# Performance work log

Measured on AMD Instinct MI355X. Metric: run time of the kernel, lower is better.

## Reference

```python
import jax, jax.numpy as jnp
import numpy as np

D = 64
H = 4
HD = D // H
N_MOL, E_MOL = 2048, 32768
N_PROT, E_PROT = 8192, 262144
LN_EPS = 1e-5


def _lin_params(key, d_in, d_out):
    k1, k2 = jax.random.split(key)
    lim = 1.0 / np.sqrt(d_in)
    w = jax.random.uniform(k1, (d_in, d_out), minval=-lim, maxval=lim, dtype=jnp.float32)
    b = jax.random.uniform(k2, (d_out,), minval=-lim, maxval=lim, dtype=jnp.float32)
    return w, b


def setup_inputs() -> dict:
    key = jax.random.key(0)
    ks = jax.random.split(key, 20)
    inp = {
        'x_mol': jax.random.normal(ks[0], (N_MOL, D), dtype=jnp.float32),
        'edge_index_mol': jax.random.randint(ks[1], (2, E_MOL), 0, N_MOL),
        'edge_attr_mol': jax.random.normal(ks[2], (E_MOL, D), dtype=jnp.float32),
        'x_prot': jax.random.normal(ks[3], (N_PROT, D), dtype=jnp.float32),
        'edge_index_prot': jax.random.randint(ks[4], (2, E_PROT), 0, N_PROT),
        'edge_attr_prot': jax.random.normal(ks[5], (E_PROT, D), dtype=jnp.float32),
    }
    # GINE MLPs: Linear -> ReLU -> Linear
    inp['mol_w1'], inp['mol_b1'] = _lin_params(ks[6], D, D)
    inp['mol_w2'], inp['mol_b2'] = _lin_params(ks[7], D, D)
    inp['prot_w1'], inp['prot_b1'] = _lin_params(ks[8], D, D)
    inp['prot_w2'], inp['prot_b2'] = _lin_params(ks[9], D, D)
    # cross-attn mol->prot (query=mol, key/value=prot)
    inp['mp_wq'], inp['mp_bq'] = _lin_params(ks[10], D, D)
    inp['mp_wk'], inp['mp_bk'] = _lin_params(ks[11], D, D)
    inp['mp_wv'], inp['mp_bv'] = _lin_params(ks[12], D, D)
    # cross-attn prot->mol (query=prot, key/value=mol)
    inp['pm_wq'], inp['pm_bq'] = _lin_params(ks[13], D, D)
    inp['pm_wk'], inp['pm_bk'] = _lin_params(ks[14], D, D)
    inp['pm_wv'], inp['pm_bv'] = _lin_params(ks[15], D, D)
    # layer norms
    inp['ln_mol_g'] = jnp.ones((D,), jnp.float32)
    inp['ln_mol_b'] = jnp.zeros((D,), jnp.float32)
    inp['ln_prot_g'] = jnp.ones((D,), jnp.float32)
    inp['ln_prot_b'] = jnp.zeros((D,), jnp.float32)
    return inp


def _gine_conv(x, edge_index, edge_attr, w1, b1, w2, b2, n_nodes):
    # message: relu(x_j + edge_attr); aggregate: mean at target; update: MLP((1+eps)*x + aggr), eps=0
    src, dst = edge_index[0], edge_index[1]
    msg = jax.nn.relu(x[src] + edge_attr)                       # [E, D]
    ssum = jax.ops.segment_sum(msg, dst, num_segments=n_nodes)  # [N, D]
    cnt = jax.ops.segment_sum(jnp.ones((msg.shape[0],), msg.dtype), dst, num_segments=n_nodes)
    aggr = ssum / jnp.maximum(cnt, 1.0)[:, None]
    h = x + aggr
    h = jax.nn.relu(h @ w1 + b1) @ w2 + b2
    return h


def _cross_attn(q_nodes, k_nodes, wq, bq, wk, bk, wv, bv):
    Nq, Nk = q_nodes.shape[0], k_nodes.shape[0]
    Q = (q_nodes @ wq + bq).reshape(Nq, H, HD)
    K = (k_nodes @ wk + bk).reshape(Nk, H, HD)
    V = (k_nodes @ wv + bv).reshape(Nk, H, HD)
    scores = jnp.einsum('qhd,khd->hqk', Q, K) / np.sqrt(HD).astype(np.float32)
    attn = jax.nn.softmax(scores, axis=-1)                      # [H, Nq, Nk]
    out = jnp.einsum('hqk,khd->qhd', attn, V).reshape(Nq, D)
    return out


def _layer_norm(x, g, b):
    mu = jnp.mean(x, axis=-1, keepdims=True)
    var = jnp.mean(jnp.square(x - mu), axis=-1, keepdims=True)
    return (x - mu) * jax.lax.rsqrt(var + LN_EPS) * g + b


def reference(x_mol, edge_index_mol, edge_attr_mol, x_prot, edge_index_prot, edge_attr_prot,
              mol_w1, mol_b1, mol_w2, mol_b2, prot_w1, prot_b1, prot_w2, prot_b2,
              mp_wq, mp_bq, mp_wk, mp_bk, mp_wv, mp_bv,
              pm_wq, pm_bq, pm_wk, pm_bk, pm_wv, pm_bv,
              ln_mol_g, ln_mol_b, ln_prot_g, ln_prot_b):
    h_mol = jax.nn.relu(_gine_conv(x_mol, edge_index_mol, edge_attr_mol,
                                   mol_w1, mol_b1, mol_w2, mol_b2, x_mol.shape[0]))
    h_prot = jax.nn.relu(_gine_conv(x_prot, edge_index_prot, edge_attr_prot,
                                    prot_w1, prot_b1, prot_w2, prot_b2, x_prot.shape[0]))
    h_mol_attn = _cross_attn(h_mol, h_prot, mp_wq, mp_bq, mp_wk, mp_bk, mp_wv, mp_bv)
    h_prot_attn = _cross_attn(h_prot, h_mol, pm_wq, pm_bq, pm_wk, pm_bk, pm_wv, pm_bv)
    out_mol = _layer_norm(h_mol + h_mol_attn, ln_mol_g, ln_mol_b)
    out_prot = _layer_norm(h_prot + h_prot_attn, ln_prot_g, ln_prot_b)
    return out_mol, out_prot
```

## Files before the change

### kernel.cpp

```cpp
#include <hip/hip_runtime.h>

#define NM 2048
#define EM 32768
#define NP 8192
#define EP 262144

typedef __attribute__((ext_vector_type(8))) short short8;
typedef __attribute__((ext_vector_type(4))) float f32x4;

#define LOG2E 1.44269504088896340736f

__device__ __forceinline__ float e2(float x) { return __builtin_amdgcn_exp2f(x); }
__device__ __forceinline__ unsigned int pk_bf16(float a, float b) {
    unsigned int ua = __float_as_uint(a) + 0x8000u;
    unsigned int ub = __float_as_uint(b) + 0x8000u;
    return __builtin_amdgcn_perm(ua, ub, 0x03020706u);
}
__device__ __forceinline__ unsigned short cvt_bf16(float f) {
    unsigned int u = __float_as_uint(f);
    u = (u + 0x7fff + ((u >> 16) & 1)) >> 16;
    return (unsigned short)u;
}

__global__ __launch_bounds__(256) void hist_kernel(
    const int* __restrict__ ei_m, const int* __restrict__ ei_p,
    int* __restrict__ cnt_m, int* __restrict__ cnt_p)
{
    int idx = blockIdx.x * 256 + threadIdx.x;
    if (idx < EM) atomicAdd(&cnt_m[ei_m[EM + idx]], 1);
    int j = idx - EM;
    if (j >= 0 && j < EP) atomicAdd(&cnt_p[ei_p[EP + j]], 1);
}

__global__ __launch_bounds__(256) void scan_kernel(
    const int* __restrict__ cnt_m, const int* __restrict__ cnt_p,
    int* __restrict__ start_m, int* __restrict__ start_p,
    int* __restrict__ cur_m, int* __restrict__ cur_p)
{
    const int* cnt; int* start; int* cur; int n;
    if (blockIdx.x == 0) { cnt = cnt_m; start = start_m; cur = cur_m; n = NM; }
    else                 { cnt = cnt_p; start = start_p; cur = cur_p; n = NP; }
    int per = n >> 8;
    int tid = threadIdx.x;
    int base = tid * per;
    int s = 0;
    for (int i = 0; i < per; i++) s += cnt[base + i];
    __shared__ int wsum[4];
    int lane = tid & 63, w = tid >> 6;
    int v = s;
    #pragma unroll
    for (int off = 1; off < 64; off <<= 1) {
        int u = __shfl_up(v, off, 64);
        if (lane >= off) v += u;
    }
    if (lane == 63) wsum[w] = v;
    __syncthreads();
    int wo = 0;
    for (int i = 0; i < w; i++) wo += wsum[i];
    int run = wo + v - s;
    for (int i = 0; i < per; i++) {
        start[base + i] = run; cur[base + i] = run;
        run += cnt[base + i];
    }
    if (tid == 255) start[n] = run;
}

__global__ __launch_bounds__(256) void scatter_kernel(
    const int* __restrict__ ei_m, const int* __restrict__ ei_p,
    int* __restrict__ cur_m, int* __restrict__ cur_p,
    int* __restrict__ pidx_m, int* __restrict__ pidx_p)
{
    int idx = blockIdx.x * 256 + threadIdx.x;
    if (idx < EM) {
        int d = ei_m[EM + idx];
        int pos = atomicAdd(&cur_m[d], 1);
        pidx_m[pos] = (idx << 11) | ei_m[idx];
    }
    int j = idx - EM;
    if (j >= 0 && j < EP) {
        int d = ei_p[EP + j];
        int pos = atomicAdd(&cur_p[d], 1);
        pidx_p[pos] = (j << 13) | ei_p[j];
    }
}

__global__ __launch_bounds__(256) void node_aggr_kernel(
    const float* __restrict__ x_m, const float* __restrict__ ea_m,
    const int* __restrict__ start_m, const int* __restrict__ pidx_m,
    const float* __restrict__ x_p, const float* __restrict__ ea_p,
    const int* __restrict__ start_p, const int* __restrict__ pidx_p,
    float* __restrict__ h0_m, float* __restrict__ h0_p)
{
    int wave = threadIdx.x >> 6, lane = threadIdx.x & 63;
    int nid = blockIdx.x * 4 + wave;
    const float *x, *ea; const int *start, *pidx; float* h0; int n, sh, msk;
    if (nid < NM) { x = x_m; ea = ea_m; start = start_m; pidx = pidx_m; h0 = h0_m; n = nid; sh = 11; msk = 2047; }
    else          { x = x_p; ea = ea_p; start = start_p; pidx = pidx_p; h0 = h0_p; n = nid - NM; sh = 13; msk = 8191; }
    int b = start[n], e = start[n + 1];
    int deg = e - b;
    float acc = 0.f;
    for (int c0 = 0; c0 < deg; c0 += 64) {
        int rem = deg - c0;
        int mcount = rem < 64 ? rem : 64;
        int pk = 0;
        if (lane < mcount) pk = pidx[b + c0 + lane];
        int j = 0;
        for (; j + 3 < mcount; j += 4) {
            int v0 = __shfl(pk, j, 64),     v1 = __shfl(pk, j + 1, 64);
            int v2 = __shfl(pk, j + 2, 64), v3 = __shfl(pk, j + 3, 64);
            float a0 = ea[(size_t)(((unsigned)v0) >> sh) * 64 + lane];
            float a1 = ea[(size_t)(((unsigned)v1) >> sh) * 64 + lane];
            float a2 = ea[(size_t)(((unsigned)v2) >> sh) * 64 + lane];
            float a3 = ea[(size_t)(((unsigned)v3) >> sh) * 64 + lane];
            float y0 = x[(size_t)(v0 & msk) * 64 + lane];
            float y1 = x[(size_t)(v1 & msk) * 64 + lane];
            float y2 = x[(size_t)(v2 & msk) * 64 + lane];
            float y3 = x[(size_t)(v3 & msk) * 64 + lane];
            acc += fmaxf(y0 + a0, 0.f);
            acc += fmaxf(y1 + a1, 0.f);
            acc += fmaxf(y2 + a2, 0.f);
            acc += fmaxf(y3 + a3, 0.f);
        }
        for (; j < mcount; ++j) {
            int v0 = __shfl(pk, j, 64);
            acc += fmaxf(x[(size_t)(v0 & msk) * 64 + lane] + ea[(size_t)(((unsigned)v0) >> sh) * 64 + lane], 0.f);
        }
    }
    float aggr = acc / fmaxf((float)deg, 1.f);
    h0[(size_t)n * 64 + lane] = x[(size_t)n * 64 + lane] + aggr;
}

__global__ __launch_bounds__(256) void gine_mlp_kernel(
    const float* __restrict__ h0_m, const float* __restrict__ h0_p,
    const float* __restrict__ w1m, const float* __restrict__ b1m,
    const float* __restrict__ w2m, const float* __restrict__ b2m,
    const float* __restrict__ w1p, const float* __restrict__ b1p,
    const float* __restrict__ w2p, const float* __restrict__ b2p,
    float* __restrict__ hm, float* __restrict__ hp)
{
    const float *h0, *w1, *b1, *w2, *b2; float* out; int row0;
    if (blockIdx.x < NM / 16) {
        h0 = h0_m; w1 = w1m; b1 = b1m; w2 = w2m; b2 = b2m; out = hm;
        row0 = blockIdx.x * 16;
    } else {
        h0 = h0_p; w1 = w1p; b1 = b1p; w2 = w2p; b2 = b2p; out = hp;
        row0 = (blockIdx.x - NM / 16) * 16;
    }
    __shared__ float sW1[4096], sW2[4096], sb1[64], sb2[64];
    __shared__ float sh0[16][64], sh1[16][64];
    int t = threadIdx.x;
    for (int i = t; i < 4096; i += 256) { sW1[i] = w1[i]; sW2[i] = w2[i]; }
    if (t < 64) { sb1[t] = b1[t]; sb2[t] = b2[t]; }
    for (int i = t; i < 16 * 64; i += 256) {
        int r = i >> 6, c = i & 63;
        sh0[r][c] = h0[(size_t)(row0 + r) * 64 + c];
    }
    __syncthreads();
    int j = t & 63, rs = t >> 6;
    for (int r = rs; r < 16; r += 4) {
        float a = sb1[j];
        #pragma unroll
        for (int c = 0; c < 64; c++) a += sh0[r][c] * sW1[c * 64 + j];
        sh1[r][j] = fmaxf(a, 0.0f);
    }
    __syncthreads();
    for (int r = rs; r < 16; r += 4) {
        float a = sb2[j];
        #pragma unroll
        for (int c = 0; c < 64; c++) a += sh1[r][c] * sW2[c * 64 + j];
        out[(size_t)(row0 + r) * 64 + j] = fmaxf(a, 0.0f);
    }
}

__global__ __launch_bounds__(256) void qkv_bf16_kernel(
    const float* __restrict__ hm, const float* __restrict__ hp,
    const float* __restrict__ wq_m, const float* __restrict__ bq_m,
    const float* __restrict__ wk_m, const float* __restrict__ bk_m,
    const float* __restrict__ wv_m, const float* __restrict__ bv_m,
    const float* __restrict__ wq_p, const float* __restrict__ bq_p,
    const float* __restrict__ wk_p, const float* __restrict__ bk_p,
    const float* __restrict__ wv_p, const float* __restrict__ bv_p,
    unsigned short* __restrict__ Qm, unsigned short* __restrict__ Km, unsigned short* __restrict__ Vtm,
    unsigned short* __restrict__ Qp, unsigned short* __restrict__ Kp, unsigned short* __restrict__ Vtp)
{
    const float *x, *wq, *bq, *wk, *bk, *wv, *bv;
    unsigned short *Q, *K, *Vt; int row0, N;
    if (blockIdx.x < NM / 16) {
        x = hm; wq = wq_m; bq = bq_m; wk = wk_m; bk = bk_m; wv = wv_m; bv = bv_m;
        Q = Qm; K = Km; Vt = Vtm; N = NM; row0 = blockIdx.x * 16;
    } else {
        x = hp; wq = wq_p; bq = bq_p; wk = wk_p; bk = bk_p; wv = wv_p; bv = bv_p;
        Q = Qp; K = Kp; Vt = Vtp; N = NP; row0 = (blockIdx.x - NM / 16) * 16;
    }
    __shared__ float sWq[4096], sWk[4096], sWv[4096];
    __shared__ float sbq[64], sbk[64], sbv[64];
    __shared__ float sh0[16][64];
    int t = threadIdx.x;
    for (int i = t; i < 4096; i += 256) { sWq[i] = wq[i]; sWk[i] = wk[i]; sWv[i] = wv[i]; }
    if (t < 64) { sbq[t] = bq[t]; sbk[t] = bk[t]; sbv[t] = bv[t]; }
    for (int i = t; i < 16 * 64; i += 256) {
        int r = i >> 6, c = i & 63;
        sh0[r][c] = x[(size_t)(row0 + r) * 64 + c];
    }
    __syncthreads();
    int j = t & 63, rs = t >> 6;
    for (int r = rs; r < 16; r += 4) {
        float aq = sbq[j], ak = sbk[j], av = sbv[j];
        #pragma unroll
        for (int c = 0; c < 64; c++) {
            float h = sh0[r][c];
            aq += h * sWq[c * 64 + j];
            ak += h * sWk[c * 64 + j];
            av += h * sWv[c * 64 + j];
        }
        size_t o = (size_t)(row0 + r) * 64 + j;
        Q[o] = cvt_bf16(aq * (0.25f * LOG2E));
        K[o] = cvt_bf16(ak);
        Vt[(size_t)j * N + row0 + r] = cvt_bf16(av);
    }
}

__global__ __launch_bounds__(256) void attn_kernel(
    const unsigned short* __restrict__ Qm, const unsigned short* __restrict__ Km,
    const unsigned short* __restrict__ Vtm,
    const unsigned short* __restrict__ Qp, const unsigned short* __restrict__ Kp,
    const unsigned short* __restrict__ Vtp,
    float* __restrict__ partial)
{
    __shared__ unsigned int plds[4][16][20];
    int t = threadIdx.x;
    int wave = t >> 6;
    int lane = t & 63;
    int qrow = lane & 15;
    int quad = lane >> 4;
    int T = blockIdx.x * 4 + wave;

    const unsigned short *Q, *K, *Vt; int Nk, ncb, tloc;
    if (T < 4096) { Q = Qm; K = Kp; Vt = Vtp; Nk = NP; ncb = 3; tloc = T; }
    else          { Q = Qp; K = Km; Vt = Vtm; Nk = NM; ncb = 1; tloc = T - 4096; }
    int chunk = tloc & ((1 << ncb) - 1);
    int tmp = tloc >> ncb;
    int h = tmp & 3;
    int qt = tmp >> 2;

    short8 qf = {};
    if (quad < 2)
        qf = *(const short8*)(Q + ((size_t)(qt * 16 + qrow)) * 64 + h * 16 + quad * 8);

    float m = -3.0e38f, l = 0.0f;
    f32x4 acc = {0.f, 0.f, 0.f, 0.f};
    const f32x4 zero4 = {0.f, 0.f, 0.f, 0.f};
    int kbase = chunk * 1024;
    const unsigned short* vrow = Vt + ((size_t)(h * 16 + qrow)) * Nk;

    short8 kf0n = {}, kf1n = {}, vfn;
    {
        if (quad < 2) {
            kf0n = *(const short8*)(K + ((size_t)(kbase + qrow)) * 64 + h * 16 + quad * 8);
            kf1n = *(const short8*)(K + ((size_t)(kbase + 16 + qrow)) * 64 + h * 16 + quad * 8);
        }
        vfn = *(const short8*)(vrow + kbase + quad * 8);
    }

    for (int it = 0; it < 32; ++it) {
        short8 kf0 = kf0n, kf1 = kf1n, vf = vfn;
        if (it < 31) {
            int key0 = kbase + (it + 1) * 32;
            if (quad < 2) {
                kf0n = *(const short8*)(K + ((size_t)(key0 + qrow)) * 64 + h * 16 + quad * 8);
                kf1n = *(const short8*)(K + ((size_t)(key0 + 16 + qrow)) * 64 + h * 16 + quad * 8);
            }
            vfn = *(const short8*)(vrow + key0 + quad * 8);
        }

        f32x4 s0 = __builtin_amdgcn_mfma_f32_16x16x32_bf16(kf0, qf, zero4, 0, 0, 0);
        f32x4 s1 = __builtin_amdgcn_mfma_f32_16x16x32_bf16(kf1, qf, zero4, 0, 0, 0);

        float tmax = fmaxf(fmaxf(fmaxf(s0.x, s0.y), fmaxf(s0.z, s0.w)),
                           fmaxf(fmaxf(s1.x, s1.y), fmaxf(s1.z, s1.w)));
        tmax = fmaxf(tmax, __shfl_xor(tmax, 16, 64));
        tmax = fmaxf(tmax, __shfl_xor(tmax, 32, 64));
        float mnew = fmaxf(m, tmax);
        float alpha = e2(m - mnew);
        float p00 = e2(s0.x - mnew), p01 = e2(s0.y - mnew);
        float p02 = e2(s0.z - mnew), p03 = e2(s0.w - mnew);
        float p10 = e2(s1.x - mnew), p11 = e2(s1.y - mnew);
        float p12 = e2(s1.z - mnew), p13 = e2(s1.w - mnew);
        l = l * alpha + (((p00 + p01) + (p02 + p03)) + ((p10 + p11) + (p12 + p13)));
        acc.x *= alpha; acc.y *= alpha; acc.z *= alpha; acc.w *= alpha;

        uint2 w0; w0.x = pk_bf16(p00, p01); w0.y = pk_bf16(p02, p03);
        uint2 w1; w1.x = pk_bf16(p10, p11); w1.y = pk_bf16(p12, p13);
        *(uint2*)&plds[wave][qrow][quad * 2] = w0;
        *(uint2*)&plds[wave][qrow][8 + quad * 2] = w1;
        short8 pf = *(short8*)&plds[wave][qrow][quad * 4];

        acc = __builtin_amdgcn_mfma_f32_16x16x32_bf16(vf, pf, acc, 0, 0, 0);
        m = mnew;
    }

    float ltot = l + __shfl_xor(l, 16, 64);
    ltot += __shfl_xor(ltot, 32, 64);

    float* pb = partial + (size_t)T * 288;
    *(f32x4*)&pb[qrow * 16 + quad * 4] = acc;
    if (quad == 0) { pb[256 + qrow] = m; pb[272 + qrow] = ltot; }
}

__global__ __launch_bounds__(256) void merge_ln_kernel(
    const float* __restrict__ partial,
    const float* __restrict__ h_m, const float* __restrict__ h_p,
    const float* __restrict__ gm, const float* __restrict__ bm,
    const float* __restrict__ gp, const float* __restrict__ bp_,
    float* __restrict__ out)
{
    int t = threadIdx.x;
    int grow = blockIdx.x * 4 + (t >> 6);
    int c = t & 63;
    const float *pbase, *hbuf, *g, *bb; float* o; int NC, row;
    if (grow < NM) { pbase = partial;               hbuf = h_m; g = gm; bb = bm;  o = out;             NC = 8; row = grow; }
    else           { pbase = partial + 4096 * 288;  hbuf = h_p; g = gp; bb = bp_; o = out + NM * 64;   NC = 2; row = grow - NM; }
    int hi = c >> 4, d = c & 15;
    int qt = row >> 4, ql = row & 15;
    const float* base = pbase + (size_t)(qt * 4 + hi) * NC * 288;
    float M = -3.0e38f;
    for (int cc = 0; cc < NC; ++cc) M = fmaxf(M, base[cc * 288 + 256 + ql]);
    float L = 0.0f, A = 0.0f;
    for (int cc = 0; cc < NC; ++cc) {
        float w = e2(base[cc * 288 + 256 + ql] - M);
        L += base[cc * 288 + 272 + ql] * w;
        A += base[cc * 288 + ql * 16 + d] * w;
    }
    float v = hbuf[(size_t)row * 64 + c] + A / L;
    float s = v;
    #pragma unroll
    for (int o2 = 32; o2 >= 1; o2 >>= 1) s += __shfl_xor(s, o2, 64);
    float mu = s * (1.0f / 64.0f);
    float dv = v - mu;
    float sq = dv * dv;
    #pragma unroll
    for (int o2 = 32; o2 >= 1; o2 >>= 1) sq += __shfl_xor(sq, o2, 64);
    float var = sq * (1.0f / 64.0f);
    o[(size_t)row * 64 + c] = dv * rsqrtf(var + 1e-5f) * g[c] + bb[c];
}

extern "C" void kernel_launch(void* const* d_in, const int* in_sizes, int n_in,
                              void* d_out, int out_size, void* d_ws, size_t ws_size,
                              hipStream_t stream)
{
    const float* x_mol   = (const float*)d_in[0];
    const int*   ei_mol  = (const int*)  d_in[1];
    const float* ea_mol  = (const float*)d_in[2];
    const float* x_prot  = (const float*)d_in[3];
    const int*   ei_prot = (const int*)  d_in[4];
    const float* ea_prot = (const float*)d_in[5];
    const float* mol_w1  = (const float*)d_in[6];
    const float* mol_b1  = (const float*)d_in[7];
    const float* mol_w2  = (const float*)d_in[8];
    const float* mol_b2  = (const float*)d_in[9];
    const float* prot_w1 = (const float*)d_in[10];
    const float* prot_b1 = (const float*)d_in[11];
    const float* prot_w2 = (const float*)d_in[12];
    const float* prot_b2 = (const float*)d_in[13];
    const float* mp_wq = (const float*)d_in[14]; const float* mp_bq = (const float*)d_in[15];
    const float* mp_wk = (const float*)d_in[16]; const float* mp_bk = (const float*)d_in[17];
    const float* mp_wv = (const float*)d_in[18]; const float* mp_bv = (const float*)d_in[19];
    const float* pm_wq = (const float*)d_in[20]; const float* pm_bq = (const float*)d_in[21];
    const float* pm_wk = (const float*)d_in[22]; const float* pm_bk = (const float*)d_in[23];
    const float* pm_wv = (const float*)d_in[24]; const float* pm_bv = (const float*)d_in[25];
    const float* ln_mol_g  = (const float*)d_in[26];
    const float* ln_mol_b  = (const float*)d_in[27];
    const float* ln_prot_g = (const float*)d_in[28];
    const float* ln_prot_b = (const float*)d_in[29];

    float* ws = (float*)d_ws;
    float* h_mol   = ws;
    float* h_prot  = h_mol + 131072;
    float* partial = h_prot + 524288;
    float* h0_mol  = partial;
    float* h0_prot = h0_mol + 131072;
    int* ip      = (int*)(partial + 2359296);
    int* cnt_m   = ip;
    int* cnt_p   = cnt_m + 2048;
    int* start_m = cnt_p + 8192;
    int* start_p = start_m + 2052;
    int* cur_m   = start_p + 8196;
    int* cur_p   = cur_m + 2048;
    int* pidx_m  = cur_p + 8192;
    int* pidx_p  = pidx_m + 32768;
    unsigned short* bf = (unsigned short*)(pidx_p + 262144);
    unsigned short* Qm  = bf;
    unsigned short* Km  = Qm + 131072;
    unsigned short* Vtm = Km + 131072;
    unsigned short* Qp  = Vtm + 131072;
    unsigned short* Kp  = Qp + 524288;
    unsigned short* Vtp = Kp + 524288;

    hipMemsetAsync(cnt_m, 0, (size_t)(2048 + 8192) * sizeof(int), stream);

    const int EB = (EM + EP) / 256;
    hist_kernel<<<EB, 256, 0, stream>>>(ei_mol, ei_prot, cnt_m, cnt_p);
    scan_kernel<<<2, 256, 0, stream>>>(cnt_m, cnt_p, start_m, start_p, cur_m, cur_p);
    scatter_kernel<<<EB, 256, 0, stream>>>(ei_mol, ei_prot, cur_m, cur_p, pidx_m, pidx_p);
    node_aggr_kernel<<<(NM + NP) / 4, 256, 0, stream>>>(
        x_mol, ea_mol, start_m, pidx_m,
        x_prot, ea_prot, start_p, pidx_p, h0_mol, h0_prot);

    gine_mlp_kernel<<<(NM + NP) / 16, 256, 0, stream>>>(
        h0_mol, h0_prot, mol_w1, mol_b1, mol_w2, mol_b2,
        prot_w1, prot_b1, prot_w2, prot_b2, h_mol, h_prot);

    qkv_bf16_kernel<<<(NM + NP) / 16, 256, 0, stream>>>(
        h_mol, h_prot,
        mp_wq, mp_bq, pm_wk, pm_bk, pm_wv, pm_bv,
        pm_wq, pm_bq, mp_wk, mp_bk, mp_wv, mp_bv,
        Qm, Km, Vtm, Qp, Kp, Vtp);

    attn_kernel<<<2048, 256, 0, stream>>>(Qm, Km, Vtm, Qp, Kp, Vtp, partial);

    float* out = (float*)d_out;
    merge_ln_kernel<<<(NM + NP) / 4, 256, 0, stream>>>(
        partial, h_mol, h_prot, ln_mol_g, ln_mol_b, ln_prot_g, ln_prot_b, out);
}
```

Measured before the change: 323.3 us.

## Use Cauchy-Schwarz static softmax max, deeper K/V prefetch, float4 edge gather

Node aggregation now processes four edges per wave at once with float4 loads per lane, then reduces across lane groups, replacing the per-lane scalar gather. The QKV kernel computes per-row Q and K norms and atomically records global maxima. Attention uses the product of those maxima as a fixed softmax offset, removing the online max, rescaling and cross-lane max shuffles. K/V prefetch is deepened to two stages with double-buffered P in LDS. The fixed offset is a loose upper bound and can cause exp underflow in bf16 and fp32 when scores sit far below it, which risks accuracy, and it adds atomics plus a global dependency between kernels.

```diff
diff --git a/kernel.cpp b/kernel.cpp
--- a/kernel.cpp
+++ b/kernel.cpp
@@ -92,42 +92,44 @@
     float* __restrict__ h0_m, float* __restrict__ h0_p)
 {
     int wave = threadIdx.x >> 6, lane = threadIdx.x & 63;
+    int slot = lane >> 4, dq = lane & 15;
     int nid = blockIdx.x * 4 + wave;
     const float *x, *ea; const int *start, *pidx; float* h0; int n, sh, msk;
     if (nid < NM) { x = x_m; ea = ea_m; start = start_m; pidx = pidx_m; h0 = h0_m; n = nid; sh = 11; msk = 2047; }
     else          { x = x_p; ea = ea_p; start = start_p; pidx = pidx_p; h0 = h0_p; n = nid - NM; sh = 13; msk = 8191; }
     int b = start[n], e = start[n + 1];
     int deg = e - b;
-    float acc = 0.f;
-    for (int c0 = 0; c0 < deg; c0 += 64) {
-        int rem = deg - c0;
-        int mcount = rem < 64 ? rem : 64;
-        int pk = 0;
-        if (lane < mcount) pk = pidx[b + c0 + lane];
-        int j = 0;
-        for (; j + 3 < mcount; j += 4) {
-            int v0 = __shfl(pk, j, 64),     v1 = __shfl(pk, j + 1, 64);
-            int v2 = __shfl(pk, j + 2, 64), v3 = __shfl(pk, j + 3, 64);
-            float a0 = ea[(size_t)(((unsigned)v0) >> sh) * 64 + lane];
-            float a1 = ea[(size_t)(((unsigned)v1) >> sh) * 64 + lane];
-            float a2 = ea[(size_t)(((unsigned)v2) >> sh) * 64 + lane];
-            float a3 = ea[(size_t)(((unsigned)v3) >> sh) * 64 + lane];
-            float y0 = x[(size_t)(v0 & msk) * 64 + lane];
-            float y1 = x[(size_t)(v1 & msk) * 64 + lane];
-            float y2 = x[(size_t)(v2 & msk) * 64 + lane];
-            float y3 = x[(size_t)(v3 & msk) * 64 + lane];
-            acc += fmaxf(y0 + a0, 0.f);
-            acc += fmaxf(y1 + a1, 0.f);
-            acc += fmaxf(y2 + a2, 0.f);
-            acc += fmaxf(y3 + a3, 0.f);
+    const int* pp = pidx + b;
+    float4 acc = {0.f, 0.f, 0.f, 0.f};
+    for (int j = 0; j < deg; j += 4) {
+        int jj = j + slot;
+        if (jj < deg) {
+            int v = pp[jj];
+            const float4 a = *(const float4*)(ea + (size_t)(((unsigned)v) >> sh) * 64 + dq * 4);
+            const float4 y = *(const float4*)(x + (size_t)(v & msk) * 64 + dq * 4);
+            acc.x += fmaxf(y.x + a.x, 0.f);
+            acc.y += fmaxf(y.y + a.y, 0.f);
+            acc.z += fmaxf(y.z + a.z, 0.f);
+            acc.w += fmaxf(y.w + a.w, 0.f);
         }
-        for (; j < mcount; ++j) {
-            int v0 = __shfl(pk, j, 64);
-            acc += fmaxf(x[(size_t)(v0 & msk) * 64 + lane] + ea[(size_t)(((unsigned)v0) >> sh) * 64 + lane], 0.f);
-        }
-    }
-    float aggr = acc / fmaxf((float)deg, 1.f);
-    h0[(size_t)n * 64 + lane] = x[(size_t)n * 64 + lane] + aggr;
+    }
+    #pragma unroll
+    for (int off = 16; off <= 32; off <<= 1) {
+        acc.x += __shfl_xor(acc.x, off, 64);
+        acc.y += __shfl_xor(acc.y, off, 64);
+        acc.z += __shfl_xor(acc.z, off, 64);
+        acc.w += __shfl_xor(acc.w, off, 64);
+    }
+    if (slot == 0) {
+        float dinv = 1.0f / fmaxf((float)deg, 1.0f);
+        const float4 xv = *(const float4*)(x + (size_t)n * 64 + dq * 4);
+        float4 o;
+        o.x = xv.x + acc.x * dinv;
+        o.y = xv.y + acc.y * dinv;
+        o.z = xv.z + acc.z * dinv;
+        o.w = xv.w + acc.w * dinv;
+        *(float4*)(h0 + (size_t)n * 64 + dq * 4) = o;
+    }
 }
 
 __global__ __launch_bounds__(256) void gine_mlp_kernel(
@@ -181,20 +183,22 @@
     const float* __restrict__ wk_p, const float* __restrict__ bk_p,
     const float* __restrict__ wv_p, const float* __restrict__ bv_p,
     unsigned short* __restrict__ Qm, unsigned short* __restrict__ Km, unsigned short* __restrict__ Vtm,
-    unsigned short* __restrict__ Qp, unsigned short* __restrict__ Kp, unsigned short* __restrict__ Vtp)
+    unsigned short* __restrict__ Qp, unsigned short* __restrict__ Kp, unsigned short* __restrict__ Vtp,
+    int* __restrict__ norms)
 {
     const float *x, *wq, *bq, *wk, *bk, *wv, *bv;
-    unsigned short *Q, *K, *Vt; int row0, N;
+    unsigned short *Q, *K, *Vt; int row0, N, nbase;
     if (blockIdx.x < NM / 16) {
         x = hm; wq = wq_m; bq = bq_m; wk = wk_m; bk = bk_m; wv = wv_m; bv = bv_m;
-        Q = Qm; K = Km; Vt = Vtm; N = NM; row0 = blockIdx.x * 16;
+        Q = Qm; K = Km; Vt = Vtm; N = NM; row0 = blockIdx.x * 16; nbase = 0;
     } else {
         x = hp; wq = wq_p; bq = bq_p; wk = wk_p; bk = bk_p; wv = wv_p; bv = bv_p;
-        Q = Qp; K = Kp; Vt = Vtp; N = NP; row0 = (blockIdx.x - NM / 16) * 16;
+        Q = Qp; K = Kp; Vt = Vtp; N = NP; row0 = (blockIdx.x - NM / 16) * 16; nbase = 2;
     }
     __shared__ float sWq[4096], sWk[4096], sWv[4096];
     __shared__ float sbq[64], sbk[64], sbv[64];
     __shared__ float sh0[16][64];
+    __shared__ float rmx[8];
     int t = threadIdx.x;
     for (int i = t; i < 4096; i += 256) { sWq[i] = wq[i]; sWk[i] = wk[i]; sWv[i] = wv[i]; }
     if (t < 64) { sbq[t] = bq[t]; sbk[t] = bk[t]; sbv[t] = bv[t]; }
@@ -204,6 +208,7 @@
     }
     __syncthreads();
     int j = t & 63, rs = t >> 6;
+    float qmx = 0.f, kmx = 0.f;
     for (int r = rs; r < 16; r += 4) {
         float aq = sbq[j], ak = sbk[j], av = sbv[j];
         #pragma unroll
@@ -213,10 +218,29 @@
             ak += h * sWk[c * 64 + j];
             av += h * sWv[c * 64 + j];
         }
+        float qs = aq * (0.25f * LOG2E);
         size_t o = (size_t)(row0 + r) * 64 + j;
-        Q[o] = cvt_bf16(aq * (0.25f * LOG2E));
+        Q[o] = cvt_bf16(qs);
         K[o] = cvt_bf16(ak);
         Vt[(size_t)j * N + row0 + r] = cvt_bf16(av);
+        float qsq = qs * qs, ksq = ak * ak;
+        #pragma unroll
+        for (int o2 = 1; o2 <= 8; o2 <<= 1) {
+            qsq += __shfl_xor(qsq, o2, 64);
+            ksq += __shfl_xor(ksq, o2, 64);
+        }
+        qmx = fmaxf(qmx, qsq);
+        kmx = fmaxf(kmx, ksq);
+    }
+    qmx = fmaxf(qmx, __shfl_xor(qmx, 16, 64)); qmx = fmaxf(qmx, __shfl_xor(qmx, 32, 64));
+    kmx = fmaxf(kmx, __shfl_xor(kmx, 16, 64)); kmx = fmaxf(kmx, __shfl_xor(kmx, 32, 64));
+    if (j == 0) { rmx[rs] = qmx; rmx[4 + rs] = kmx; }
+    __syncthreads();
+    if (t == 0) {
+        float q4 = fmaxf(fmaxf(rmx[0], rmx[1]), fmaxf(rmx[2], rmx[3]));
+        float k4 = fmaxf(fmaxf(rmx[4], rmx[5]), fmaxf(rmx[6], rmx[7]));
+        atomicMax(&norms[nbase],     __float_as_int(sqrtf(q4)));
+        atomicMax(&norms[nbase + 1], __float_as_int(sqrtf(k4)));
     }
 }
 
@@ -225,9 +249,9 @@
     const unsigned short* __restrict__ Vtm,
     const unsigned short* __restrict__ Qp, const unsigned short* __restrict__ Kp,
     const unsigned short* __restrict__ Vtp,
-    float* __restrict__ partial)
-{
-    __shared__ unsigned int plds[4][16][20];
+    const int* __restrict__ norms, float* __restrict__ partial)
+{
+    __shared__ unsigned int plds[4][2][16][20];
     int t = threadIdx.x;
     int wave = t >> 6;
     int lane = t & 63;
@@ -235,9 +259,11 @@
     int quad = lane >> 4;
     int T = blockIdx.x * 4 + wave;
 
-    const unsigned short *Q, *K, *Vt; int Nk, ncb, tloc;
-    if (T < 4096) { Q = Qm; K = Kp; Vt = Vtp; Nk = NP; ncb = 3; tloc = T; }
-    else          { Q = Qp; K = Km; Vt = Vtm; Nk = NM; ncb = 1; tloc = T - 4096; }
+    const unsigned short *Q, *K, *Vt; int Nk, ncb, tloc; float m;
+    if (T < 4096) { Q = Qm; K = Kp; Vt = Vtp; Nk = NP; ncb = 3; tloc = T;
+                    m = __int_as_float(norms[0]) * __int_as_float(norms[3]); }
+    else          { Q = Qp; K = Km; Vt = Vtm; Nk = NM; ncb = 1; tloc = T - 4096;
+                    m = __int_as_float(norms[2]) * __int_as_float(norms[1]); }
     int chunk = tloc & ((1 << ncb) - 1);
     int tmp = tloc >> ncb;
     int h = tmp & 3;
@@ -247,56 +273,53 @@
     if (quad < 2)
         qf = *(const short8*)(Q + ((size_t)(qt * 16 + qrow)) * 64 + h * 16 + quad * 8);
 
-    float m = -3.0e38f, l = 0.0f;
-    f32x4 acc = {0.f, 0.f, 0.f, 0.f};
     const f32x4 zero4 = {0.f, 0.f, 0.f, 0.f};
     int kbase = chunk * 1024;
-    const unsigned short* vrow = Vt + ((size_t)(h * 16 + qrow)) * Nk;
-
-    short8 kf0n = {}, kf1n = {}, vfn;
-    {
+    const unsigned short* krow = K + (size_t)(kbase + qrow) * 64 + h * 16 + quad * 8;
+    const unsigned short* vrow = Vt + ((size_t)(h * 16 + qrow)) * Nk + kbase + quad * 8;
+
+    float l = 0.0f;
+    f32x4 acc = zero4;
+
+    short8 kf0p[2], kf1p[2], vfp[2];
+    #pragma unroll
+    for (int i = 0; i < 2; ++i) {
+        kf0p[i] = (short8){}; kf1p[i] = (short8){};
         if (quad < 2) {
-            kf0n = *(const short8*)(K + ((size_t)(kbase + qrow)) * 64 + h * 16 + quad * 8);
-            kf1n = *(const short8*)(K + ((size_t)(kbase + 16 + qrow)) * 64 + h * 16 + quad * 8);
+            kf0p[i] = *(const short8*)(krow + (size_t)(i * 32) * 64);
+            kf1p[i] = *(const short8*)(krow + (size_t)(i * 32 + 16) * 64);
         }
-        vfn = *(const short8*)(vrow + kbase + quad * 8);
-    }
-
+        vfp[i] = *(const short8*)(vrow + i * 32);
+    }
+
+    #pragma unroll 2
     for (int it = 0; it < 32; ++it) {
-        short8 kf0 = kf0n, kf1 = kf1n, vf = vfn;
-        if (it < 31) {
-            int key0 = kbase + (it + 1) * 32;
+        short8 kf0 = kf0p[it & 1], kf1 = kf1p[it & 1], vf = vfp[it & 1];
+        if (it < 30) {
+            int off = (it + 2) * 32;
             if (quad < 2) {
-                kf0n = *(const short8*)(K + ((size_t)(key0 + qrow)) * 64 + h * 16 + quad * 8);
-                kf1n = *(const short8*)(K + ((size_t)(key0 + 16 + qrow)) * 64 + h * 16 + quad * 8);
+                kf0p[it & 1] = *(const short8*)(krow + (size_t)off * 64);
+                kf1p[it & 1] = *(const short8*)(krow + (size_t)(off + 16) * 64);
             }
-            vfn = *(const short8*)(vrow + key0 + quad * 8);
+            vfp[it & 1] = *(const short8*)(vrow + off);
         }
 
         f32x4 s0 = __builtin_amdgcn_mfma_f32_16x16x32_bf16(kf0, qf, zero4, 0, 0, 0);
         f32x4 s1 = __builtin_amdgcn_mfma_f32_16x16x32_bf16(kf1, qf, zero4, 0, 0, 0);
 
-        float tmax = fmaxf(fmaxf(fmaxf(s0.x, s0.y), fmaxf(s0.z, s0.w)),
-                           fmaxf(fmaxf(s1.x, s1.y), fmaxf(s1.z, s1.w)));
-        tmax = fmaxf(tmax, __shfl_xor(tmax, 16, 64));
-        tmax = fmaxf(tmax, __shfl_xor(tmax, 32, 64));
-        float mnew = fmaxf(m, tmax);
-        float alpha = e2(m - mnew);
-        float p00 = e2(s0.x - mnew), p01 = e2(s0.y - mnew);
-        float p02 = e2(s0.z - mnew), p03 = e2(s0.w - mnew);
-        float p10 = e2(s1.x - mnew), p11 = e2(s1.y - mnew);
-        float p12 = e2(s1.z - mnew), p13 = e2(s1.w - mnew);
-        l = l * alpha + (((p00 + p01) + (p02 + p03)) + ((p10 + p11) + (p12 + p13)));
-        acc.x *= alpha; acc.y *= alpha; acc.z *= alpha; acc.w *= alpha;
+        float p00 = e2(s0.x - m), p01 = e2(s0.y - m);
+        float p02 = e2(s0.z - m), p03 = e2(s0.w - m);
+        float p10 = e2(s1.x - m), p11 = e2(s1.y - m);
+        float p12 = e2(s1.z - m), p13 = e2(s1.w - m);
+        l += (((p00 + p01) + (p02 + p03)) + ((p10 + p11) + (p12 + p13)));
 
         uint2 w0; w0.x = pk_bf16(p00, p01); w0.y = pk_bf16(p02, p03);
         uint2 w1; w1.x = pk_bf16(p10, p11); w1.y = pk_bf16(p12, p13);
-        *(uint2*)&plds[wave][qrow][quad * 2] = w0;
-        *(uint2*)&plds[wave][qrow][8 + quad * 2] = w1;
-        short8 pf = *(short8*)&plds[wave][qrow][quad * 4];
+        *(uint2*)&plds[wave][it & 1][qrow][quad * 2] = w0;
+        *(uint2*)&plds[wave][it & 1][qrow][8 + quad * 2] = w1;
+        short8 pf = *(short8*)&plds[wave][it & 1][qrow][quad * 4];
 
         acc = __builtin_amdgcn_mfma_f32_16x16x32_bf16(vf, pf, acc, 0, 0, 0);
-        m = mnew;
     }
 
     float ltot = l + __shfl_xor(l, 16, 64);
@@ -382,7 +405,8 @@
     int* ip      = (int*)(partial + 2359296);
     int* cnt_m   = ip;
     int* cnt_p   = cnt_m + 2048;
-    int* start_m = cnt_p + 8192;
+    int* norms   = cnt_p + 8192;
+    int* start_m = norms + 4;
     int* start_p = start_m + 2052;
     int* cur_m   = start_p + 8196;
     int* cur_p   = cur_m + 2048;
@@ -396,7 +420,7 @@
     unsigned short* Kp  = Qp + 524288;
     unsigned short* Vtp = Kp + 524288;
 
-    hipMemsetAsync(cnt_m, 0, (size_t)(2048 + 8192) * sizeof(int), stream);
+    hipMemsetAsync(cnt_m, 0, (size_t)(2048 + 8192 + 4) * sizeof(int), stream);
 
     const int EB = (EM + EP) / 256;
     hist_kernel<<<EB, 256, 0, stream>>>(ei_mol, ei_prot, cnt_m, cnt_p);
@@ -414,9 +438,9 @@
         h_mol, h_prot,
         mp_wq, mp_bq, pm_wk, pm_bk, pm_wv, pm_bv,
         pm_wq, pm_bq, mp_wk, mp_bk, mp_wv, mp_bv,
-        Qm, Km, Vtm, Qp, Kp, Vtp);
-
-    attn_kernel<<<2048, 256, 0, stream>>>(Qm, Km, Vtm, Qp, Kp, Vtp, partial);
+        Qm, Km, Vtm, Qp, Kp, Vtp, norms);
+
+    attn_kernel<<<2048, 256, 0, stream>>>(Qm, Km, Vtm, Qp, Kp, Vtp, norms, partial);
 
     float* out = (float*)d_out;
     merge_ln_kernel<<<(NM + NP) / 4, 256, 0, stream>>>(
```

New measurement: 336.7 us. 4.2% more time.
